# Kernel tuning notes

Measured on AMD Instinct MI355X. Metric: run time of the kernel, lower is better.

The kernel has to match this reference:

```python
import jax, jax.numpy as jnp
import numpy as np

B = 1024      # number of states
NP = 32       # SVGD particles per state
AD = 20       # act_dim
OD = 64       # obs_dim
H = 256       # critic hidden width
STEPS = 5     # num_svgd_steps
LR = 0.1      # svgd_lr (adaptive_lr disabled)
SP0 = 1.0     # svgd_sigma_p0
ALIM = 1.0    # act_limit


def _q(obs, X, w1, b1, w2, b2, w3, b3):
    h = jnp.concatenate([obs, X], axis=-1)
    h = jax.nn.relu(h @ w1 + b1)
    h = jax.nn.relu(h @ w2 + b2)
    return jnp.squeeze(h @ w3 + b3, -1)


def _rbf(X):
    # X: [B, NP, AD] -> K [B,NP,NP], diff [B,NP,NP,AD], gamma [B,1,1], K_grad [B,NP,NP,AD]
    diff = X[:, :, None, :] - X[:, None, :, :]
    dist_sq = jnp.sum(diff * diff, axis=-1)
    # adaptive bandwidth via median heuristic (adaptive_sig=True)
    med = jnp.median(dist_sq.reshape(dist_sq.shape[0], -1), axis=-1)
    sig_sq = med / (2.0 * jnp.log(NP + 1.0))
    gamma = (1.0 / (2.0 * sig_sq + 1e-8))[:, None, None]
    K = jnp.exp(-gamma * dist_sq)
    K_grad = -2.0 * gamma[..., None] * diff * K[..., None]  # d/dx_i K(x_i, x_j)
    return K, diff, gamma, K_grad


def setup_inputs():
    key = jax.random.key(0)
    ks = jax.random.split(key, 16)
    N = B * NP

    def lin(k, fi, fo):
        return (jax.random.normal(k, (fi, fo), jnp.float32) / np.sqrt(fi)).astype(jnp.float32)

    return {
        "obs": jax.random.normal(ks[0], (N, OD), jnp.float32),
        "a0": jax.random.normal(ks[1], (N, AD), jnp.float32) * np.sqrt(SP0),
        "q1_w1": lin(ks[2], OD + AD, H), "q1_b1": jnp.zeros((H,), jnp.float32),
        "q1_w2": lin(ks[3], H, H),       "q1_b2": jnp.zeros((H,), jnp.float32),
        "q1_w3": lin(ks[4], H, 1),       "q1_b3": jnp.zeros((1,), jnp.float32),
        "q2_w1": lin(ks[5], OD + AD, H), "q2_b1": jnp.zeros((H,), jnp.float32),
        "q2_w2": lin(ks[6], H, H),       "q2_b2": jnp.zeros((H,), jnp.float32),
        "q2_w3": lin(ks[7], H, 1),       "q2_b3": jnp.zeros((1,), jnp.float32),
    }


def reference(obs, a0, q1_w1, q1_b1, q1_w2, q1_b2, q1_w3, q1_b3,
              q2_w1, q2_b1, q2_w2, q2_b2, q2_w3, q2_b3):
    eye = jnp.eye(NP, dtype=a0.dtype)

    def q_min_sum(Xf):
        q1 = _q(obs, Xf, q1_w1, q1_b1, q1_w2, q1_b2, q1_w3, q1_b3)
        q2 = _q(obs, Xf, q2_w1, q2_b1, q2_w2, q2_b2, q2_w3, q2_b3)
        return jnp.sum(jnp.minimum(q1, q2))

    score_fn = jax.grad(q_min_sum)  # autograd score function

    def step(carry, _):
        a, logp = carry
        score = score_fn(a).reshape(-1, NP, AD)                 # [B,NP,AD]
        X = a.reshape(-1, NP, AD)
        K, diff, gamma, Kg = _rbf(X)
        phi = (jnp.einsum('bij,bjd->bid', K, score) + Kg.sum(axis=1)) / NP
        # log-prob correction terms (with_logprob=True)
        term1 = jnp.mean(jnp.sum(Kg * score[:, None, :, :], axis=-1), axis=2)     # [B,NP]
        inner = jnp.sum(jnp.transpose(Kg, (0, 2, 1, 3)) * diff, axis=-1) \
                - AD * (K - eye)
        term2 = -2.0 * gamma[:, :, 0] * jnp.mean(inner, axis=1)                   # [B,NP]
        logp = logp - LR * (term1 + term2)
        a = a + LR * phi.reshape(a.shape)                        # svgd_optim
        return (a, logp), None

    logp0 = jnp.zeros((B, NP), a0.dtype)
    (a, logp_svgd), _ = jax.lax.scan(step, (a0, logp0), None, length=STEPS)

    a_sq = ALIM * jnp.tanh(a)                                    # [B*NP, AD]
    logp_normal = (-AD * 0.5 * jnp.log(2.0 * jnp.pi * SP0)
                   - 0.5 / SP0 * jnp.sum(a0 * a0, axis=-1)).reshape(-1, NP)
    logp_tanh = -jnp.sum(2.0 * (jnp.log(2.0) - a - jax.nn.softplus(-2.0 * a)),
                         axis=-1).reshape(-1, NP)
    logp_a = jnp.mean(logp_normal + logp_svgd + logp_tanh, axis=-1)  # [B]
    return a_sq, logp_a
```

## Files before the change

kernel.cpp:

```cpp
#include <hip/hip_runtime.h>
#include <math.h>

#define NPART 32
#define ADIM  20
#define ODIM  64
#define HID   256
#define NSTEPS 5
#define LRC   0.1f
#define NBLK  512
#define LOG33 3.4965075614664802f

typedef short bf8 __attribute__((ext_vector_type(8)));
typedef float f4  __attribute__((ext_vector_type(4)));

#define OW1T(n) ((n)*24576)
#define OW2T(n) (49152 + (n)*65536)
#define OW2C(n) (180224 + (n)*65536)
#define OW1X(n) (311296 + (n)*8192)
#define OW3B(n) (327680 + (n)*256)
#define WS_ELEMS 328192

__device__ __forceinline__ short f2bf(float x) {
    unsigned u = __float_as_uint(x);
    u += 0x7FFFu + ((u >> 16) & 1u);
    return (short)(u >> 16);
}
__device__ __forceinline__ short f2bfT(float x) {
    return (short)(__float_as_uint(x) >> 16);
}
__device__ __forceinline__ float bf2f(short s) {
    return __uint_as_float(((unsigned)(unsigned short)s) << 16);
}

#define MFMA(a,b,c) __builtin_amdgcn_mfma_f32_16x16x32_bf16((a),(b),(c),0,0,0)

__global__ void prep_weights(const float* __restrict__ w1a, const float* __restrict__ w2a,
                             const float* __restrict__ w3a, const float* __restrict__ w1b,
                             const float* __restrict__ w2b, const float* __restrict__ w3b,
                             unsigned short* __restrict__ ws)
{
    int idx = blockIdx.x * 256 + threadIdx.x;
    if (idx >= WS_ELEMS) return;
    float val;
    if (idx < 49152) {
        int net = idx / 24576, rem = idx % 24576;
        int n = rem / 96, k = rem % 96;
        const float* w1 = net ? w1b : w1a;
        val = (k < 84) ? w1[k*256 + n] : 0.f;
    } else if (idx < 180224) {
        int t2 = idx - 49152; int net = t2 / 65536, rem = t2 % 65536;
        int n = rem / 256, k = rem % 256;
        const float* w2 = net ? w2b : w2a;
        val = w2[k*256 + n];
    } else if (idx < 311296) {
        int t2 = idx - 180224; int net = t2 / 65536, rem = t2 % 65536;
        const float* w2 = net ? w2b : w2a;
        val = w2[rem];
    } else if (idx < 327680) {
        int t2 = idx - 311296; int net = t2 / 8192, rem = t2 % 8192;
        int d = rem / 256, n = rem % 256;
        const float* w1 = net ? w1b : w1a;
        val = (d < 20) ? w1[(64 + d)*256 + n] : 0.f;
    } else {
        int t2 = idx - 327680; int net = t2 / 256, k = t2 % 256;
        const float* w3 = net ? w3b : w3a;
        val = w3[k];
    }
    ws[idx] = (unsigned short)f2bf(val);
}

__global__ void __launch_bounds__(512, 4)
svgd_main(const float* __restrict__ obs,  const float* __restrict__ a0g,
          const float* __restrict__ b1a,  const float* __restrict__ b2a, const float* __restrict__ b3a,
          const float* __restrict__ b1b,  const float* __restrict__ b2b, const float* __restrict__ b3b,
          const float* __restrict__ w3af, const float* __restrict__ w3bf,
          const unsigned short* __restrict__ ws, float* __restrict__ out)
{
    __shared__ __align__(16) short A0s[64*96];
    __shared__ __align__(16) short hbuf[64*264];
    __shared__ unsigned maskS[2][2][64][8];
    __shared__ float Xm[64*20];
    __shared__ float scoreS[64*21];
    __shared__ float qpart[2][8][64];
    __shared__ int   winsS[64];
    __shared__ float logps[64];
    __shared__ unsigned short lutI[496], lutJ[496];
    __shared__ float med2[4];
    __shared__ float qvS[64];
    __shared__ float normsS[64], diagS[64], rowKS[64];

    float* d2sF = (float*)hbuf;
    float* GSF  = ((float*)hbuf) + 2048;
    short* KbS  = hbuf + 8192;
    short* SBs  = hbuf + 10240;
    short* STbS = hbuf + 12288;
    short* XTbS = hbuf + 14336;

    const int t = threadIdx.x, b = blockIdx.x;
    const int lane = t & 63, wv = t >> 6;
    const int q = lane >> 4, mp = lane & 15;
    const int nb = wv * 32;

    for (int p = t; p < 64*ODIM; p += 512) {
        int i = p >> 6, d = p & 63;
        A0s[i*96 + d] = f2bfT(obs[(b*64 + i)*ODIM + d]);
    }
    for (int p = t; p < 64*ADIM; p += 512) {
        int i = p / 20, d = p - i*20;
        float v = a0g[(b*64 + i)*20 + d];
        Xm[p] = v;
        A0s[i*96 + 64 + d] = f2bfT(v);
    }
    for (int p = t; p < 64*12; p += 512) { int i = p/12, d = p - i*12; A0s[i*96 + 84 + d] = 0; }
    { unsigned* mz = &maskS[0][0][0][0];
      for (int p = t; p < 2*2*64*8; p += 512) mz[p] = 0u; }
    if (t < 496) {
        int i_ = 0, rem = t;
        while (rem >= 31 - i_) { rem -= 31 - i_; ++i_; }
        lutI[t] = (unsigned short)i_; lutJ[t] = (unsigned short)(i_ + 1 + rem);
    }
    if (t < 64) logps[t] = 0.f;
    __syncthreads();

    for (int step = 0; step < NSTEPS; ++step) {
        for (int net = 0; net < 2; ++net) {
            const unsigned short* w1t = ws + OW1T(net);
            const unsigned short* w2t = ws + OW2T(net);
            const float* b1p = net ? b1b : b1a;
            const float* b2p = net ? b2b : b2a;
            const float* w3p = net ? w3bf : w3af;

            f4 acc[4][2];
            #pragma unroll
            for (int h = 0; h < 4; ++h) { acc[h][0] = (f4){0,0,0,0}; acc[h][1] = (f4){0,0,0,0}; }
            {
                const unsigned short* bp0 = w1t + (size_t)(nb +      mp)*96 + q*8;
                const unsigned short* bp1 = w1t + (size_t)(nb + 16 + mp)*96 + q*8;
                bf8 bb0 = *(const bf8*)bp0, bb1 = *(const bf8*)bp1;
                #pragma unroll
                for (int k0 = 0; k0 < 96; k0 += 32) {
                    bf8 n0 = bb0, n1 = bb1;
                    if (k0 + 32 < 96) { n0 = *(const bf8*)(bp0 + k0 + 32); n1 = *(const bf8*)(bp1 + k0 + 32); }
                    #pragma unroll
                    for (int h = 0; h < 4; ++h) {
                        bf8 aa = *(const bf8*)&A0s[(h*16 + mp)*96 + k0 + q*8];
                        acc[h][0] = MFMA(aa, bb0, acc[h][0]);
                        acc[h][1] = MFMA(aa, bb1, acc[h][1]);
                    }
                    bb0 = n0; bb1 = n1;
                }
            }
            #pragma unroll
            for (int h = 0; h < 4; ++h) {
                #pragma unroll
                for (int s = 0; s < 2; ++s) {
                    int n0 = nb + s*16, col = n0 + mp;
                    float bias = b1p[col];
                    #pragma unroll
                    for (int r = 0; r < 4; ++r) {
                        float v = acc[h][s][r] + bias;
                        bool pos = v > 0.f;
                        unsigned long long bal = __ballot(pos);
                        hbuf[(h*16 + q*4 + r)*264 + col] = f2bfT(pos ? v : 0.f);
                        if (mp == 0)
                            atomicOr(&maskS[net][0][h*16 + q*4 + r][n0 >> 5],
                                     ((unsigned)((bal >> (q*16)) & 0xFFFFull)) << (n0 & 16));
                    }
                }
            }
            __syncthreads();

            #pragma unroll
            for (int h = 0; h < 4; ++h) { acc[h][0] = (f4){0,0,0,0}; acc[h][1] = (f4){0,0,0,0}; }
            {
                const unsigned short* bp0 = w2t + (size_t)(nb +      mp)*256 + q*8;
                const unsigned short* bp1 = w2t + (size_t)(nb + 16 + mp)*256 + q*8;
                bf8 bb0 = *(const bf8*)bp0, bb1 = *(const bf8*)bp1;
                #pragma unroll
                for (int k0 = 0; k0 < 256; k0 += 32) {
                    bf8 n0 = bb0, n1 = bb1;
                    if (k0 + 32 < 256) { n0 = *(const bf8*)(bp0 + k0 + 32); n1 = *(const bf8*)(bp1 + k0 + 32); }
                    #pragma unroll
                    for (int h = 0; h < 4; ++h) {
                        bf8 aa = *(const bf8*)&hbuf[(h*16 + mp)*264 + k0 + q*8];
                        acc[h][0] = MFMA(aa, bb0, acc[h][0]);
                        acc[h][1] = MFMA(aa, bb1, acc[h][1]);
                    }
                    bb0 = n0; bb1 = n1;
                }
            }
            {
                float qp[4][4] = {{0,0,0,0},{0,0,0,0},{0,0,0,0},{0,0,0,0}};
                #pragma unroll
                for (int h = 0; h < 4; ++h) {
                    #pragma unroll
                    for (int s = 0; s < 2; ++s) {
                        int n0 = nb + s*16, col = n0 + mp;
                        float bias = b2p[col], w3v = w3p[col];
                        #pragma unroll
                        for (int r = 0; r < 4; ++r) {
                            float v = acc[h][s][r] + bias;
                            bool pos = v > 0.f;
                            unsigned long long bal = __ballot(pos);
                            if (mp == 0)
                                atomicOr(&maskS[net][1][h*16 + q*4 + r][n0 >> 5],
                                         ((unsigned)((bal >> (q*16)) & 0xFFFFull)) << (n0 & 16));
                            qp[h][r] += pos ? v * w3v : 0.f;
                        }
                    }
                }
                #pragma unroll
                for (int d = 1; d < 16; d <<= 1)
                    #pragma unroll
                    for (int h = 0; h < 4; ++h)
                        #pragma unroll
                        for (int r = 0; r < 4; ++r)
                            qp[h][r] += __shfl_xor(qp[h][r], d, 64);
                if (mp == 0) {
                    #pragma unroll
                    for (int h = 0; h < 4; ++h)
                        #pragma unroll
                        for (int r = 0; r < 4; ++r)
                            qpart[net][wv][h*16 + q*4 + r] = qp[h][r];
                }
            }
            __syncthreads();
        }

        if (t < 64) {
            float q0 = b3a[0], q1 = b3b[0];
            #pragma unroll
            for (int w = 0; w < 8; ++w) { q0 += qpart[0][w][t]; q1 += qpart[1][w][t]; }
            winsS[t] = (q0 <= q1) ? 0 : 1;
        }
        __syncthreads();

        for (int net = 0; net < 2; ++net) {
            const unsigned short* w2c  = ws + OW2C(net);
            const unsigned short* w3b8 = ws + OW3B(net);

            f4 acc[4][2];
            #pragma unroll
            for (int h = 0; h < 4; ++h) { acc[h][0] = (f4){0,0,0,0}; acc[h][1] = (f4){0,0,0,0}; }
            int win[4];
            #pragma unroll
            for (int h = 0; h < 4; ++h) win[h] = (winsS[h*16 + mp] == net);
            {
                const unsigned short* bp0 = w2c + (size_t)(nb +      mp)*256 + q*8;
                const unsigned short* bp1 = w2c + (size_t)(nb + 16 + mp)*256 + q*8;
                bf8 bb0 = *(const bf8*)bp0, bb1 = *(const bf8*)bp1;
                #pragma unroll
                for (int k0 = 0; k0 < 256; k0 += 32) {
                    bf8 n0 = bb0, n1 = bb1;
                    if (k0 + 32 < 256) { n0 = *(const bf8*)(bp0 + k0 + 32); n1 = *(const bf8*)(bp1 + k0 + 32); }
                    bf8 w3v = *(const bf8*)(w3b8 + k0 + q*8);
                    #pragma unroll
                    for (int h = 0; h < 4; ++h) {
                        unsigned bits = win[h] ? ((maskS[net][1][h*16 + mp][k0 >> 5] >> (q*8)) & 0xFFu) : 0u;
                        bf8 aa;
                        #pragma unroll
                        for (int j = 0; j < 8; ++j)
                            aa[j] = ((bits >> j) & 1u) ? w3v[j] : (short)0;
                        acc[h][0] = MFMA(aa, bb0, acc[h][0]);
                        acc[h][1] = MFMA(aa, bb1, acc[h][1]);
                    }
                    bb0 = n0; bb1 = n1;
                }
            }
            #pragma unroll
            for (int h = 0; h < 4; ++h) {
                #pragma unroll
                for (int s = 0; s < 2; ++s) {
                    int col = nb + s*16 + mp;
                    #pragma unroll
                    for (int r = 0; r < 4; ++r) {
                        int row = h*16 + q*4 + r;
                        bool on = (maskS[net][0][row][col >> 5] >> (col & 31)) & 1u;
                        hbuf[row*264 + col] = f2bfT(on ? acc[h][s][r] : 0.f);
                    }
                }
            }
            __syncthreads();
            {
                int mt = wv & 3, ch = wv >> 2;
                const unsigned short* w1x = ws + OW1X(net);
                const unsigned short* bp  = w1x + (size_t)(ch*16 + mp)*256 + q*8;
                f4 sa = (f4){0,0,0,0};
                bf8 bx = *(const bf8*)bp;
                #pragma unroll
                for (int k0 = 0; k0 < 256; k0 += 32) {
                    bf8 nx = bx;
                    if (k0 + 32 < 256) nx = *(const bf8*)(bp + k0 + 32);
                    bf8 aa = *(const bf8*)&hbuf[(mt*16 + mp)*264 + k0 + q*8];
                    sa = MFMA(aa, bx, sa);
                    bx = nx;
                }
                int colD = ch*16 + mp;
                if (colD < 20) {
                    #pragma unroll
                    for (int r = 0; r < 4; ++r) {
                        int row = mt*16 + q*4 + r;
                        if (net == 0) scoreS[row*21 + colD]  = sa[r];
                        else          scoreS[row*21 + colD] += sa[r];
                    }
                }
            }
            __syncthreads();
        }

        if (t < 64) {
            int st = t >> 5;
            float nrm = 0.f, dg = 0.f;
            #pragma unroll
            for (int d = 0; d < 20; ++d) {
                float xb = bf2f(A0s[t*96 + 64 + d]);
                nrm += xb * xb;
                float sv = scoreS[t*21 + d];
                float xv = Xm[t*20 + d];
                dg += xv * sv;
                short sb = f2bfT(sv);
                SBs[t*32 + d] = sb;
                STbS[st*1024 + d*32 + (t & 31)] = sb;
                XTbS[st*1024 + d*32 + (t & 31)] = f2bfT(xv);
            }
            #pragma unroll
            for (int d = 20; d < 32; ++d) SBs[t*32 + d] = 0;
            normsS[t] = nrm;
            diagS[t]  = dg;
        }
        __syncthreads();

        {
            int stw = wv >> 2, mt = (wv >> 1) & 1, nt = wv & 1;
            bf8 aa  = *(const bf8*)&A0s[(stw*32 + mt*16 + mp)*96 + 64 + q*8];
            bf8 bbx = *(const bf8*)&A0s[(stw*32 + nt*16 + mp)*96 + 64 + q*8];
            bf8 bbs = *(const bf8*)&SBs[(stw*32 + nt*16 + mp)*32 + q*8];
            f4 gx = MFMA(aa, bbx, ((f4){0,0,0,0}));
            f4 gs = MFMA(aa, bbs, ((f4){0,0,0,0}));
            int jl = nt*16 + mp;
            float nj = normsS[stw*32 + jl];
            #pragma unroll
            for (int r = 0; r < 4; ++r) {
                int il = mt*16 + q*4 + r;
                d2sF[stw*1024 + il*32 + jl] = normsS[stw*32 + il] + nj - 2.f*gx[r];
                GSF [stw*1024 + il*32 + jl] = gs[r];
            }
        }
        __syncthreads();

        if (wv < 2) {
            const float* base = d2sF + wv*1024;
            float v[8];
            #pragma unroll
            for (int i = 0; i < 8; ++i) {
                int e = lane*8 + i;
                v[i] = (e < 496) ? base[lutI[e]*32 + lutJ[e]] : 3.4e38f;
            }
            for (int k = 2; k <= 512; k <<= 1) {
                for (int jj = k >> 1; jj >= 8; jj >>= 1) {
                    int lm = jj >> 3;
                    #pragma unroll
                    for (int i = 0; i < 8; ++i) {
                        float w = __shfl_xor(v[i], lm, 64);
                        int p = lane*8 + i;
                        bool takeMin = (((p & k) == 0) == ((p & jj) == 0));
                        v[i] = takeMin ? fminf(v[i], w) : fmaxf(v[i], w);
                    }
                }
                int jj0 = (k >> 1) < 4 ? (k >> 1) : 4;
                for (int jj = jj0; jj >= 1; jj >>= 1) {
                    #pragma unroll
                    for (int i = 0; i < 8; ++i) {
                        if ((i & jj) == 0) {
                            int i2 = i | jj;
                            int p = lane*8 + i;
                            bool up = ((p & k) == 0);
                            float x = v[i], y = v[i2];
                            float mn = fminf(x, y), mx = fmaxf(x, y);
                            v[i] = up ? mn : mx; v[i2] = up ? mx : mn;
                        }
                    }
                }
            }
            if (lane == 29) med2[wv*2 + 0] = v[7];
            if (lane == 30) med2[wv*2 + 1] = v[0];
        } else {
            unsigned* mz = &maskS[0][0][0][0];
            for (int p = t - 128; p < 2*2*64*8; p += 384) mz[p] = 0u;
        }
        __syncthreads();

        {
            int i = t >> 3, stw = i >> 5, il = i & 31, j0 = (t & 7) * 4;
            float medv = 0.5f * (med2[stw*2] + med2[stw*2 + 1]);
            float gam  = 1.f / (2.f * (medv / (2.f * LOG33)) + 1e-8f);
            float sK = 0.f, sKGS = 0.f, sKd2 = 0.f, sKdg = 0.f;
            #pragma unroll
            for (int jj = 0; jj < 4; ++jj) {
                int j = j0 + jj;
                float d2 = d2sF[stw*1024 + il*32 + j];
                float K  = expf(-gam * d2);
                KbS[stw*1024 + il*32 + j] = f2bfT(K);
                sK   += K;
                sKGS += K * GSF[stw*1024 + il*32 + j];
                sKd2 += K * d2;
                sKdg += K * diagS[stw*32 + j];
            }
            #pragma unroll
            for (int d = 1; d < 8; d <<= 1) {
                sK   += __shfl_xor(sK,   d, 64);
                sKGS += __shfl_xor(sKGS, d, 64);
                sKd2 += __shfl_xor(sKd2, d, 64);
                sKdg += __shfl_xor(sKdg, d, 64);
            }
            if ((t & 7) == 0) {
                rowKS[i] = sK;
                float sdots = sKGS - sKdg;
                float ssum  = -2.f*gam*sdots
                              - 2.f*gam*(2.f*gam*sKd2 - 20.f*(sK - 1.f));
                logps[i] -= LRC * (ssum * (1.f/32.f));
            }
        }
        __syncthreads();

        {
            int stw = wv >> 2, mt = (wv >> 1) & 1, nt = wv & 1;
            float medv = 0.5f * (med2[stw*2] + med2[stw*2 + 1]);
            float gam  = 1.f / (2.f * (medv / (2.f * LOG33)) + 1e-8f);
            bf8 aa  = *(const bf8*)&KbS [stw*1024 + (mt*16 + mp)*32 + q*8];
            bf8 b1v = *(const bf8*)&STbS[stw*1024 + (nt*16 + mp)*32 + q*8];
            bf8 b2v = *(const bf8*)&XTbS[stw*1024 + (nt*16 + mp)*32 + q*8];
            f4 ks = MFMA(aa, b1v, ((f4){0,0,0,0}));
            f4 kx = MFMA(aa, b2v, ((f4){0,0,0,0}));
            int dd = nt*16 + mp;
            if (dd < 20) {
                #pragma unroll
                for (int r = 0; r < 4; ++r) {
                    int gi = stw*32 + mt*16 + q*4 + r;
                    float xi  = Xm[gi*20 + dd];
                    float phi = (ks[r] + 2.f*gam*(xi*rowKS[gi] - kx[r])) * (1.f/32.f);
                    float nx  = xi + LRC * phi;
                    Xm[gi*20 + dd] = nx;
                    A0s[gi*96 + 64 + dd] = f2bfT(nx);
                }
            }
        }
        __syncthreads();
    }

    for (int p = t; p < 64*20; p += 512) {
        int i = p / 20, d = p - i*20;
        out[(b*64 + i)*20 + d] = tanhf(Xm[p]);
    }
    if (t < 64) {
        float lt = 0.f, s0 = 0.f;
        for (int d = 0; d < 20; ++d) {
            float a  = Xm[t*20 + d];
            float x  = -2.f * a;
            float sp = fmaxf(x, 0.f) + log1pf(expf(-fabsf(x)));
            lt -= 2.f * (0.69314718056f - a - sp);
            float v = a0g[(b*64 + t)*20 + d];
            s0 += v * v;
        }
        qvS[t] = -18.3787706641f - 0.5f*s0 + logps[t] + lt;
    }
    __syncthreads();
    if (t < 2) {
        float s = 0.f;
        for (int i = 0; i < 32; ++i) s += qvS[t*32 + i];
        out[1024*32*20 + b*2 + t] = s * (1.f/32.f);
    }
}

extern "C" void kernel_launch(void* const* d_in, const int* in_sizes, int n_in,
                              void* d_out, int out_size, void* d_ws, size_t ws_size,
                              hipStream_t stream) {
    unsigned short* ws = (unsigned short*)d_ws;
    prep_weights<<<(WS_ELEMS + 255)/256, 256, 0, stream>>>(
        (const float*)d_in[2],  (const float*)d_in[4],  (const float*)d_in[6],
        (const float*)d_in[8],  (const float*)d_in[10], (const float*)d_in[12], ws);
    svgd_main<<<NBLK, 512, 0, stream>>>(
        (const float*)d_in[0],  (const float*)d_in[1],
        (const float*)d_in[3],  (const float*)d_in[5],  (const float*)d_in[7],
        (const float*)d_in[9],  (const float*)d_in[11], (const float*)d_in[13],
        (const float*)d_in[6],  (const float*)d_in[12],
        ws, (float*)d_out);
}
```

Before: 495.4 us.

## Pad LDS layouts, fold w3 into W2, and replace atomic mask writes

Pads the A0s, d2/GS and K/score/X tile row strides in shared memory to cut LDS bank conflicts. W3 is pre-multiplied into the transposed W2 copy during weight prep, so the backward mask operand becomes a 0/1 bf16 pattern taken from a 16-entry lookup table instead of per-element selects. Mask words are written directly once per wave instead of with atomicOr, which also removes the per-step mask zeroing. The K-row reduction is vectorized with float4 loads. Folding w3 into bf16 W2 adds a slight rounding change.

```diff
diff --git a/kernel.cpp b/kernel.cpp
--- a/kernel.cpp
+++ b/kernel.cpp
@@ -9,16 +9,18 @@
 #define LRC   0.1f
 #define NBLK  512
 #define LOG33 3.4965075614664802f
+#define A0LD  104
 
 typedef short bf8 __attribute__((ext_vector_type(8)));
+typedef short s4b __attribute__((ext_vector_type(4)));
 typedef float f4  __attribute__((ext_vector_type(4)));
+typedef unsigned u4 __attribute__((ext_vector_type(4)));
 
 #define OW1T(n) ((n)*24576)
 #define OW2T(n) (49152 + (n)*65536)
 #define OW2C(n) (180224 + (n)*65536)
 #define OW1X(n) (311296 + (n)*8192)
-#define OW3B(n) (327680 + (n)*256)
-#define WS_ELEMS 328192
+#define WS_ELEMS 327680
 
 __device__ __forceinline__ short f2bf(float x) {
     unsigned u = __float_as_uint(x);
@@ -55,16 +57,13 @@
     } else if (idx < 311296) {
         int t2 = idx - 180224; int net = t2 / 65536, rem = t2 % 65536;
         const float* w2 = net ? w2b : w2a;
-        val = w2[rem];
-    } else if (idx < 327680) {
+        const float* w3 = net ? w3b : w3a;
+        val = w2[rem] * w3[rem % 256];
+    } else {
         int t2 = idx - 311296; int net = t2 / 8192, rem = t2 % 8192;
         int d = rem / 256, n = rem % 256;
         const float* w1 = net ? w1b : w1a;
         val = (d < 20) ? w1[(64 + d)*256 + n] : 0.f;
-    } else {
-        int t2 = idx - 327680; int net = t2 / 256, k = t2 % 256;
-        const float* w3 = net ? w3b : w3a;
-        val = w3[k];
     }
     ws[idx] = (unsigned short)f2bf(val);
 }
@@ -76,7 +75,7 @@
           const float* __restrict__ w3af, const float* __restrict__ w3bf,
           const unsigned short* __restrict__ ws, float* __restrict__ out)
 {
-    __shared__ __align__(16) short A0s[64*96];
+    __shared__ __align__(16) short A0s[64*A0LD];
     __shared__ __align__(16) short hbuf[64*264];
     __shared__ unsigned maskS[2][2][64][8];
     __shared__ float Xm[64*20];
@@ -87,13 +86,15 @@
     __shared__ unsigned short lutI[496], lutJ[496];
     __shared__ float med2[4];
     __shared__ float qvS[64];
-    __shared__ float normsS[64], diagS[64], rowKS[64];
+    __shared__ float normsS[64], rowKS[64];
+    __shared__ __align__(16) float diagS[64];
+    __shared__ __align__(16) uint2 lutE[16];
 
     float* d2sF = (float*)hbuf;
-    float* GSF  = ((float*)hbuf) + 2048;
-    short* KbS  = hbuf + 8192;
-    short* SBs  = hbuf + 10240;
-    short* STbS = hbuf + 12288;
+    float* GSF  = ((float*)hbuf) + 2304;
+    short* SBs  = hbuf + 9216;
+    short* KbS  = hbuf + 9216;
+    short* STbS = hbuf + 11776;
     short* XTbS = hbuf + 14336;
 
     const int t = threadIdx.x, b = blockIdx.x;
@@ -103,21 +104,23 @@
 
     for (int p = t; p < 64*ODIM; p += 512) {
         int i = p >> 6, d = p & 63;
-        A0s[i*96 + d] = f2bfT(obs[(b*64 + i)*ODIM + d]);
+        A0s[i*A0LD + d] = f2bfT(obs[(b*64 + i)*ODIM + d]);
     }
     for (int p = t; p < 64*ADIM; p += 512) {
         int i = p / 20, d = p - i*20;
         float v = a0g[(b*64 + i)*20 + d];
         Xm[p] = v;
-        A0s[i*96 + 64 + d] = f2bfT(v);
-    }
-    for (int p = t; p < 64*12; p += 512) { int i = p/12, d = p - i*12; A0s[i*96 + 84 + d] = 0; }
-    { unsigned* mz = &maskS[0][0][0][0];
-      for (int p = t; p < 2*2*64*8; p += 512) mz[p] = 0u; }
+        A0s[i*A0LD + 64 + d] = f2bfT(v);
+    }
+    for (int p = t; p < 64*12; p += 512) { int i = p/12, d = p - i*12; A0s[i*A0LD + 84 + d] = 0; }
     if (t < 496) {
         int i_ = 0, rem = t;
         while (rem >= 31 - i_) { rem -= 31 - i_; ++i_; }
         lutI[t] = (unsigned short)i_; lutJ[t] = (unsigned short)(i_ + 1 + rem);
+    }
+    if (t < 16) {
+        lutE[t] = make_uint2(((t & 1) ? 0x3F80u : 0u) | ((t & 2) ? 0x3F800000u : 0u),
+                             ((t & 4) ? 0x3F80u : 0u) | ((t & 8) ? 0x3F800000u : 0u));
     }
     if (t < 64) logps[t] = 0.f;
     __syncthreads();
@@ -143,28 +146,32 @@
                     if (k0 + 32 < 96) { n0 = *(const bf8*)(bp0 + k0 + 32); n1 = *(const bf8*)(bp1 + k0 + 32); }
                     #pragma unroll
                     for (int h = 0; h < 4; ++h) {
-                        bf8 aa = *(const bf8*)&A0s[(h*16 + mp)*96 + k0 + q*8];
+                        bf8 aa = *(const bf8*)&A0s[(h*16 + mp)*A0LD + k0 + q*8];
                         acc[h][0] = MFMA(aa, bb0, acc[h][0]);
                         acc[h][1] = MFMA(aa, bb1, acc[h][1]);
                     }
                     bb0 = n0; bb1 = n1;
                 }
             }
-            #pragma unroll
-            for (int h = 0; h < 4; ++h) {
-                #pragma unroll
-                for (int s = 0; s < 2; ++s) {
-                    int n0 = nb + s*16, col = n0 + mp;
-                    float bias = b1p[col];
+            {
+                float bias0 = b1p[nb + mp], bias1 = b1p[nb + 16 + mp];
+                #pragma unroll
+                for (int h = 0; h < 4; ++h) {
                     #pragma unroll
                     for (int r = 0; r < 4; ++r) {
-                        float v = acc[h][s][r] + bias;
-                        bool pos = v > 0.f;
-                        unsigned long long bal = __ballot(pos);
-                        hbuf[(h*16 + q*4 + r)*264 + col] = f2bfT(pos ? v : 0.f);
-                        if (mp == 0)
-                            atomicOr(&maskS[net][0][h*16 + q*4 + r][n0 >> 5],
-                                     ((unsigned)((bal >> (q*16)) & 0xFFFFull)) << (n0 & 16));
+                        float v0 = acc[h][0][r] + bias0;
+                        float v1 = acc[h][1][r] + bias1;
+                        bool p0 = v0 > 0.f, p1 = v1 > 0.f;
+                        unsigned long long bal0 = __ballot(p0);
+                        unsigned long long bal1 = __ballot(p1);
+                        int row = h*16 + q*4 + r;
+                        hbuf[row*264 + nb +      mp] = f2bfT(p0 ? v0 : 0.f);
+                        hbuf[row*264 + nb + 16 + mp] = f2bfT(p1 ? v1 : 0.f);
+                        if (mp == 0) {
+                            unsigned w = (unsigned)((bal0 >> (q*16)) & 0xFFFFull)
+                                       | (((unsigned)((bal1 >> (q*16)) & 0xFFFFull)) << 16);
+                            maskS[net][0][row][wv] = w;
+                        }
                     }
                 }
             }
@@ -190,23 +197,24 @@
                 }
             }
             {
+                float bias0 = b2p[nb + mp], bias1 = b2p[nb + 16 + mp];
+                float w30   = w3p[nb + mp], w31   = w3p[nb + 16 + mp];
                 float qp[4][4] = {{0,0,0,0},{0,0,0,0},{0,0,0,0},{0,0,0,0}};
                 #pragma unroll
                 for (int h = 0; h < 4; ++h) {
                     #pragma unroll
-                    for (int s = 0; s < 2; ++s) {
-                        int n0 = nb + s*16, col = n0 + mp;
-                        float bias = b2p[col], w3v = w3p[col];
-                        #pragma unroll
-                        for (int r = 0; r < 4; ++r) {
-                            float v = acc[h][s][r] + bias;
-                            bool pos = v > 0.f;
-                            unsigned long long bal = __ballot(pos);
-                            if (mp == 0)
-                                atomicOr(&maskS[net][1][h*16 + q*4 + r][n0 >> 5],
-                                         ((unsigned)((bal >> (q*16)) & 0xFFFFull)) << (n0 & 16));
-                            qp[h][r] += pos ? v * w3v : 0.f;
+                    for (int r = 0; r < 4; ++r) {
+                        float v0 = acc[h][0][r] + bias0;
+                        float v1 = acc[h][1][r] + bias1;
+                        bool p0 = v0 > 0.f, p1 = v1 > 0.f;
+                        unsigned long long bal0 = __ballot(p0);
+                        unsigned long long bal1 = __ballot(p1);
+                        if (mp == 0) {
+                            unsigned w = (unsigned)((bal0 >> (q*16)) & 0xFFFFull)
+                                       | (((unsigned)((bal1 >> (q*16)) & 0xFFFFull)) << 16);
+                            maskS[net][1][h*16 + q*4 + r][wv] = w;
                         }
+                        qp[h][r] += (p0 ? v0 * w30 : 0.f) + (p1 ? v1 * w31 : 0.f);
                     }
                 }
                 #pragma unroll
@@ -236,8 +244,7 @@
         __syncthreads();
 
         for (int net = 0; net < 2; ++net) {
-            const unsigned short* w2c  = ws + OW2C(net);
-            const unsigned short* w3b8 = ws + OW3B(net);
+            const unsigned short* w2c = ws + OW2C(net);
 
             f4 acc[4][2];
             #pragma unroll
@@ -253,14 +260,13 @@
                 for (int k0 = 0; k0 < 256; k0 += 32) {
                     bf8 n0 = bb0, n1 = bb1;
                     if (k0 + 32 < 256) { n0 = *(const bf8*)(bp0 + k0 + 32); n1 = *(const bf8*)(bp1 + k0 + 32); }
-                    bf8 w3v = *(const bf8*)(w3b8 + k0 + q*8);
                     #pragma unroll
                     for (int h = 0; h < 4; ++h) {
                         unsigned bits = win[h] ? ((maskS[net][1][h*16 + mp][k0 >> 5] >> (q*8)) & 0xFFu) : 0u;
-                        bf8 aa;
-                        #pragma unroll
-                        for (int j = 0; j < 8; ++j)
-                            aa[j] = ((bits >> j) & 1u) ? w3v[j] : (short)0;
+                        uint2 lo = lutE[bits & 15u];
+                        uint2 hi = lutE[bits >> 4];
+                        u4 mw; mw[0] = lo.x; mw[1] = lo.y; mw[2] = hi.x; mw[3] = hi.y;
+                        bf8 aa = __builtin_bit_cast(bf8, mw);
                         acc[h][0] = MFMA(aa, bb0, acc[h][0]);
                         acc[h][1] = MFMA(aa, bb1, acc[h][1]);
                     }
@@ -313,18 +319,18 @@
             float nrm = 0.f, dg = 0.f;
             #pragma unroll
             for (int d = 0; d < 20; ++d) {
-                float xb = bf2f(A0s[t*96 + 64 + d]);
+                float xb = bf2f(A0s[t*A0LD + 64 + d]);
                 nrm += xb * xb;
                 float sv = scoreS[t*21 + d];
                 float xv = Xm[t*20 + d];
                 dg += xv * sv;
                 short sb = f2bfT(sv);
-                SBs[t*32 + d] = sb;
-                STbS[st*1024 + d*32 + (t & 31)] = sb;
-                XTbS[st*1024 + d*32 + (t & 31)] = f2bfT(xv);
-            }
-            #pragma unroll
-            for (int d = 20; d < 32; ++d) SBs[t*32 + d] = 0;
+                SBs[t*40 + d] = sb;
+                STbS[st*1280 + d*40 + (t & 31)] = sb;
+                XTbS[st*1280 + d*40 + (t & 31)] = f2bfT(xv);
+            }
+            #pragma unroll
+            for (int d = 20; d < 32; ++d) SBs[t*40 + d] = 0;
             normsS[t] = nrm;
             diagS[t]  = dg;
         }
@@ -332,9 +338,9 @@
 
         {
             int stw = wv >> 2, mt = (wv >> 1) & 1, nt = wv & 1;
-            bf8 aa  = *(const bf8*)&A0s[(stw*32 + mt*16 + mp)*96 + 64 + q*8];
-            bf8 bbx = *(const bf8*)&A0s[(stw*32 + nt*16 + mp)*96 + 64 + q*8];
-            bf8 bbs = *(const bf8*)&SBs[(stw*32 + nt*16 + mp)*32 + q*8];
+            bf8 aa  = *(const bf8*)&A0s[(stw*32 + mt*16 + mp)*A0LD + 64 + q*8];
+            bf8 bbx = *(const bf8*)&A0s[(stw*32 + nt*16 + mp)*A0LD + 64 + q*8];
+            bf8 bbs = *(const bf8*)&SBs[(stw*32 + nt*16 + mp)*40 + q*8];
             f4 gx = MFMA(aa, bbx, ((f4){0,0,0,0}));
             f4 gs = MFMA(aa, bbs, ((f4){0,0,0,0}));
             int jl = nt*16 + mp;
@@ -342,19 +348,19 @@
             #pragma unroll
             for (int r = 0; r < 4; ++r) {
                 int il = mt*16 + q*4 + r;
-                d2sF[stw*1024 + il*32 + jl] = normsS[stw*32 + il] + nj - 2.f*gx[r];
-                GSF [stw*1024 + il*32 + jl] = gs[r];
+                d2sF[stw*1152 + il*36 + jl] = normsS[stw*32 + il] + nj - 2.f*gx[r];
+                GSF [stw*1152 + il*36 + jl] = gs[r];
             }
         }
         __syncthreads();
 
         if (wv < 2) {
-            const float* base = d2sF + wv*1024;
+            const float* base = d2sF + wv*1152;
             float v[8];
             #pragma unroll
             for (int i = 0; i < 8; ++i) {
                 int e = lane*8 + i;
-                v[i] = (e < 496) ? base[lutI[e]*32 + lutJ[e]] : 3.4e38f;
+                v[i] = (e < 496) ? base[lutI[e]*36 + lutJ[e]] : 3.4e38f;
             }
             for (int k = 2; k <= 512; k <<= 1) {
                 for (int jj = k >> 1; jj >= 8; jj >>= 1) {
@@ -384,9 +390,6 @@
             }
             if (lane == 29) med2[wv*2 + 0] = v[7];
             if (lane == 30) med2[wv*2 + 1] = v[0];
-        } else {
-            unsigned* mz = &maskS[0][0][0][0];
-            for (int p = t - 128; p < 2*2*64*8; p += 384) mz[p] = 0u;
         }
         __syncthreads();
 
@@ -394,18 +397,17 @@
             int i = t >> 3, stw = i >> 5, il = i & 31, j0 = (t & 7) * 4;
             float medv = 0.5f * (med2[stw*2] + med2[stw*2 + 1]);
             float gam  = 1.f / (2.f * (medv / (2.f * LOG33)) + 1e-8f);
-            float sK = 0.f, sKGS = 0.f, sKd2 = 0.f, sKdg = 0.f;
-            #pragma unroll
-            for (int jj = 0; jj < 4; ++jj) {
-                int j = j0 + jj;
-                float d2 = d2sF[stw*1024 + il*32 + j];
-                float K  = expf(-gam * d2);
-                KbS[stw*1024 + il*32 + j] = f2bfT(K);
-                sK   += K;
-                sKGS += K * GSF[stw*1024 + il*32 + j];
-                sKd2 += K * d2;
-                sKdg += K * diagS[stw*32 + j];
-            }
+            f4 d2 = *(const f4*)&d2sF[stw*1152 + il*36 + j0];
+            f4 gs = *(const f4*)&GSF [stw*1152 + il*36 + j0];
+            f4 dg = *(const f4*)&diagS[stw*32 + j0];
+            float K0 = expf(-gam * d2[0]), K1 = expf(-gam * d2[1]);
+            float K2 = expf(-gam * d2[2]), K3 = expf(-gam * d2[3]);
+            s4b kb; kb[0] = f2bfT(K0); kb[1] = f2bfT(K1); kb[2] = f2bfT(K2); kb[3] = f2bfT(K3);
+            *(s4b*)&KbS[stw*1280 + il*40 + j0] = kb;
+            float sK   = K0 + K1 + K2 + K3;
+            float sKGS = K0*gs[0] + K1*gs[1] + K2*gs[2] + K3*gs[3];
+            float sKd2 = K0*d2[0] + K1*d2[1] + K2*d2[2] + K3*d2[3];
+            float sKdg = K0*dg[0] + K1*dg[1] + K2*dg[2] + K3*dg[3];
             #pragma unroll
             for (int d = 1; d < 8; d <<= 1) {
                 sK   += __shfl_xor(sK,   d, 64);
@@ -427,9 +429,9 @@
             int stw = wv >> 2, mt = (wv >> 1) & 1, nt = wv & 1;
             float medv = 0.5f * (med2[stw*2] + med2[stw*2 + 1]);
             float gam  = 1.f / (2.f * (medv / (2.f * LOG33)) + 1e-8f);
-            bf8 aa  = *(const bf8*)&KbS [stw*1024 + (mt*16 + mp)*32 + q*8];
-            bf8 b1v = *(const bf8*)&STbS[stw*1024 + (nt*16 + mp)*32 + q*8];
-            bf8 b2v = *(const bf8*)&XTbS[stw*1024 + (nt*16 + mp)*32 + q*8];
+            bf8 aa  = *(const bf8*)&KbS [stw*1280 + (mt*16 + mp)*40 + q*8];
+            bf8 b1v = *(const bf8*)&STbS[stw*1280 + (nt*16 + mp)*40 + q*8];
+            bf8 b2v = *(const bf8*)&XTbS[stw*1280 + (nt*16 + mp)*40 + q*8];
             f4 ks = MFMA(aa, b1v, ((f4){0,0,0,0}));
             f4 kx = MFMA(aa, b2v, ((f4){0,0,0,0}));
             int dd = nt*16 + mp;
@@ -441,7 +443,7 @@
                     float phi = (ks[r] + 2.f*gam*(xi*rowKS[gi] - kx[r])) * (1.f/32.f);
                     float nx  = xi + LRC * phi;
                     Xm[gi*20 + dd] = nx;
-                    A0s[gi*96 + 64 + dd] = f2bfT(nx);
+                    A0s[gi*A0LD + 64 + dd] = f2bfT(nx);
                 }
             }
         }
```

Result: slower. 813.5 us (+64.2%).
